# Kernel tuning notes

Hardware: AMD Instinct MI355X
Metric: run time of the kernel (lower is better)

Reference implementation:

```python
import jax, jax.numpy as jnp
import numpy as np

B, N, T, D, H = 8, 64, 256, 256, 8
HD = D // H


def _mlp(x, W1, b1, W2, b2):
    # torch nn.Sequential(Linear, GELU(exact), Linear); weights stored pre-transposed
    return jax.nn.gelu(x @ W1 + b1, approximate=False) @ W2 + b2


def setup_inputs() -> dict:
    key = jax.random.key(0)
    ks = jax.random.split(key, 14)
    s = 0.02
    f32 = jnp.float32
    return {
        "padded_batches": jax.random.normal(ks[0], (B, N, T, D), f32),
        "sum_token": jax.random.normal(ks[1], (B, N, 1, D), f32),
        "masks": jax.random.randint(ks[2], (B, N, T), 0, 2).astype(jnp.int32),
        "positions_3d": jax.random.normal(ks[3], (B, N, T, 3), f32),
        "Wq": jax.random.normal(ks[4], (D, D), f32) * s, "bq": jnp.zeros((D,), f32),
        "Wk": jax.random.normal(ks[5], (D, D), f32) * s, "bk": jnp.zeros((D,), f32),
        "Wv": jax.random.normal(ks[6], (D, D), f32) * s, "bv": jnp.zeros((D,), f32),
        "Bw1": jax.random.normal(ks[7], (5, 64), f32) * s, "Bb1": jnp.zeros((64,), f32),
        "Bw2": jax.random.normal(ks[8], (64, H), f32) * s, "Bb2": jnp.zeros((H,), f32),
        "Vw1": jax.random.normal(ks[9], (5, 128), f32) * s, "Vb1": jnp.zeros((128,), f32),
        "Vw2": jax.random.normal(ks[10], (128, D), f32) * s, "Vb2": jnp.zeros((D,), f32),
    }


def reference(padded_batches, sum_token, masks, positions_3d,
              Wq, bq, Wk, bk, Wv, bv,
              Bw1, Bb1, Bw2, Bb2, Vw1, Vb1, Vw2, Vb2):
    Bd, Nd, Td, Dd = padded_batches.shape
    BN = Bd * Nd
    # masked-average summary token (summary_mode='avg'): [B,N,1,D]
    w = masks[..., None].astype(padded_batches.dtype)            # [B,N,T,1]
    denom = jnp.clip(w.sum(-2, keepdims=True), 1e-6)
    summary = (padded_batches * w).sum(-2, keepdims=True) / denom
    # projections (torch Linear: x @ W.T + b; weights here pre-transposed)
    q = (padded_batches @ Wq + bq).reshape(BN, Td, H, HD).transpose(0, 2, 1, 3)  # [BN,H,T,Hd]
    k = (summary @ Wk + bk).reshape(BN, 1, H, HD).transpose(0, 2, 1, 3)          # [BN,H,1,Hd]
    v = (summary @ Wv + bv).reshape(BN, 1, H, HD).transpose(0, 2, 1, 3)
    scale = 1.0 / np.sqrt(HD).astype(np.float32)
    logits = jnp.einsum('bhtd,bhsd->bhts', q, k) * scale          # [BN,H,T,1]
    # relative positional features vs. position summary
    pos_summary = (positions_3d * w).sum(-2, keepdims=True) / denom  # [B,N,1,3]
    diff = positions_3d.reshape(BN, Td, 1, 3) - pos_summary.reshape(BN, 1, 1, 3)  # [BN,T,1,3]
    dist = jnp.linalg.norm(diff, axis=-1, keepdims=True)
    dist2 = (diff ** 2).sum(-1, keepdims=True)
    rel_feat = jnp.concatenate([diff, dist, dist2], axis=-1)      # [BN,T,1,5]
    rel_bias = _mlp(rel_feat, Bw1, Bb1, Bw2, Bb2).transpose(0, 3, 1, 2)  # [BN,H,T,1]
    logits = logits + rel_bias
    neg = jnp.finfo(jnp.float32).min
    attn_mask = jnp.where(masks.reshape(BN, 1, Td, 1) == 0, neg, 0.0)
    logits = logits + attn_mask
    attn_w = jax.nn.softmax(logits, axis=-1)                      # [BN,H,T,1]
    attn = jnp.einsum('bhts,bhsd->bhtd', attn_w, v)               # [BN,H,T,Hd]
    rel_val = _mlp(rel_feat, Vw1, Vb1, Vw2, Vb2)                  # [BN,T,1,D]
    rel_val = rel_val.reshape(BN, Td, 1, H, HD).transpose(0, 3, 1, 2, 4)  # [BN,H,T,1,Hd]
    attn = attn + (attn_w[..., None] * rel_val).sum(-2)
    out = attn.transpose(0, 2, 1, 3).reshape(Bd, Nd, Td, Dd) + padded_batches
    return out
```

## Files before the change

### kernel.cpp

```cpp
#include <hip/hip_runtime.h>
#include <hip/hip_bf16.h>
#include <math.h>


#define BN_TOT 512
#define T_DIM 256
#define D_DIM 256
#define HID 128

typedef __attribute__((ext_vector_type(8))) short short8v;
typedef __attribute__((ext_vector_type(4))) float f32x4;

static __device__ __forceinline__ ushort f2bf(float f) {
    __hip_bfloat16 h = __float2bfloat16(f);
    return *reinterpret_cast<ushort*>(&h);
}

__global__ __launch_bounds__(256) void k_prep(const float* __restrict__ Vw2,
                                              ushort* __restrict__ Vw2t) {
    const int idx = (blockIdx.x * 256 + threadIdx.x) * 4;
    const int d = idx >> 7, k = idx & 127;
    ushort4 r;
    r.x = f2bf(Vw2[(size_t)(k + 0) * D_DIM + d]);
    r.y = f2bf(Vw2[(size_t)(k + 1) * D_DIM + d]);
    r.z = f2bf(Vw2[(size_t)(k + 2) * D_DIM + d]);
    r.w = f2bf(Vw2[(size_t)(k + 3) * D_DIM + d]);
    *reinterpret_cast<ushort4*>(Vw2t + d * HID + k) = r;
}

__global__ __launch_bounds__(256, 8) void k_part(
    const float* __restrict__ x,
    const int* __restrict__ masks,
    const float* __restrict__ pos,
    float* __restrict__ part_x,
    float* __restrict__ part_cp)
{
    __shared__ float s_part[4 * 256];

    const int bid = blockIdx.x;
    const int tid = threadIdx.x;
    const int bn = bid >> 2, tg = bid & 3;
    const int t0 = tg * 64;

    const float* xb = x + ((size_t)bn * T_DIM + t0) * D_DIM;
    const int*   mb = masks + bn * T_DIM + t0;

    {
        const int dq = tid & 63, tq = tid >> 6;
        float4 a = make_float4(0.f, 0.f, 0.f, 0.f);
        #pragma unroll
        for (int i = 0; i < 16; ++i) {
            const int t = tq * 16 + i;
            float m = (float)mb[t];
            float4 xv = *reinterpret_cast<const float4*>(xb + (size_t)t * D_DIM + dq * 4);
            a.x += m * xv.x; a.y += m * xv.y; a.z += m * xv.z; a.w += m * xv.w;
        }
        *reinterpret_cast<float4*>(s_part + tq * 256 + dq * 4) = a;
    }

    if (tid < 64) {
        float m = (float)mb[tid];
        const float* pp = pos + ((size_t)bn * T_DIM + t0 + tid) * 3;
        float c = m, px = m * pp[0], py = m * pp[1], pz = m * pp[2];
        #pragma unroll
        for (int off = 32; off > 0; off >>= 1) {
            c  += __shfl_down(c,  off, 64);
            px += __shfl_down(px, off, 64);
            py += __shfl_down(py, off, 64);
            pz += __shfl_down(pz, off, 64);
        }
        if (tid == 0)
            *reinterpret_cast<float4*>(part_cp + (bn * 4 + tg) * 4) =
                make_float4(c, px, py, pz);
    }
    __syncthreads();

    float s = s_part[tid] + s_part[256 + tid] + s_part[512 + tid] + s_part[768 + tid];
    part_x[((size_t)bn * 4 + tg) * 256 + tid] = s;
}

__global__ __launch_bounds__(256, 8) void k_v(
    const float* __restrict__ part_x,
    const float* __restrict__ part_cp,
    const float* __restrict__ Wv,
    const float* __restrict__ bv,
    const float* __restrict__ Vb2,
    float* __restrict__ v_ws,
    float* __restrict__ ps_ws)
{
    __shared__ float s_sum[256];
    __shared__ float s_part[4 * 256];
    __shared__ float s_cp[16];

    const int bn = blockIdx.x, tid = threadIdx.x;

    if (tid < 16) s_cp[tid] = part_cp[bn * 16 + tid];
    const float* pb = part_x + (size_t)bn * 1024;
    float s = pb[tid] + pb[256 + tid] + pb[512 + tid] + pb[768 + tid];
    __syncthreads();

    const float cnt = s_cp[0] + s_cp[4] + s_cp[8] + s_cp[12];
    const float inv = 1.0f / fmaxf(cnt, 1e-6f);
    s_sum[tid] = s * inv;
    if (tid < 3) {
        float p = s_cp[tid + 1] + s_cp[tid + 5] + s_cp[tid + 9] + s_cp[tid + 13];
        ps_ws[bn * 4 + tid] = p * inv;
    }
    __syncthreads();

    {
        const int dq = tid & 63, kq = tid >> 6;
        float4 a = make_float4(0.f, 0.f, 0.f, 0.f);
        #pragma unroll 8
        for (int i = 0; i < 64; ++i) {
            const int k = kq * 64 + i;
            float sc = s_sum[k];
            float4 w = *reinterpret_cast<const float4*>(Wv + (size_t)k * D_DIM + dq * 4);
            a.x += sc * w.x; a.y += sc * w.y; a.z += sc * w.z; a.w += sc * w.w;
        }
        *reinterpret_cast<float4*>(s_part + kq * 256 + dq * 4) = a;
    }
    __syncthreads();
    v_ws[bn * D_DIM + tid] = s_part[tid] + s_part[256 + tid] + s_part[512 + tid] +
                             s_part[768 + tid] + bv[tid] + Vb2[tid];
}

__global__ __launch_bounds__(512, 8) void k_sum(
    const float* __restrict__ x, const int* __restrict__ masks,
    const float* __restrict__ pos, const float* __restrict__ Wv,
    const float* __restrict__ bv, const float* __restrict__ Vb2,
    float* __restrict__ v_ws, float* __restrict__ ps_ws)
{
    __shared__ float s_m[256];
    __shared__ float s_red[4 * 256];
    __shared__ float s_part[8 * 256];
    __shared__ float s_sum[256];

    const int bn = blockIdx.x, tid = threadIdx.x;
    const float* xb = x + (size_t)bn * T_DIM * D_DIM;

    if (tid < 256) {
        float m = (float)masks[bn * T_DIM + tid];
        s_m[tid] = m;
        const float* pp = pos + ((size_t)bn * T_DIM + tid) * 3;
        s_red[0 * 256 + tid] = m;
        s_red[1 * 256 + tid] = m * pp[0];
        s_red[2 * 256 + tid] = m * pp[1];
        s_red[3 * 256 + tid] = m * pp[2];
    }
    __syncthreads();
    {
        const int dq = tid & 63, tq = tid >> 6;
        float4 a = make_float4(0.f, 0.f, 0.f, 0.f);
        const float* px = xb + (size_t)tq * 32 * D_DIM + dq * 4;
        #pragma unroll 8
        for (int i = 0; i < 32; ++i) {
            float m = s_m[tq * 32 + i];
            float4 xv = *reinterpret_cast<const float4*>(px + i * D_DIM);
            a.x += m * xv.x; a.y += m * xv.y; a.z += m * xv.z; a.w += m * xv.w;
        }
        *reinterpret_cast<float4*>(s_part + tq * 256 + dq * 4) = a;
    }
    __syncthreads();
    for (int off = 128; off > 0; off >>= 1) {
        if (tid < off) {
            s_red[0 * 256 + tid] += s_red[0 * 256 + tid + off];
            s_red[1 * 256 + tid] += s_red[1 * 256 + tid + off];
            s_red[2 * 256 + tid] += s_red[2 * 256 + tid + off];
            s_red[3 * 256 + tid] += s_red[3 * 256 + tid + off];
        }
        __syncthreads();
    }
    const float inv = 1.0f / fmaxf(s_red[0], 1e-6f);
    if (tid < 3) ps_ws[bn * 4 + tid] = s_red[(tid + 1) * 256] * inv;
    if (tid < 256) {
        float s = 0.f;
        #pragma unroll
        for (int q = 0; q < 8; ++q) s += s_part[q * 256 + tid];
        s_sum[tid] = s * inv;
    }
    __syncthreads();
    {
        const int dq = tid & 63, kq = tid >> 6;
        float4 a = make_float4(0.f, 0.f, 0.f, 0.f);
        #pragma unroll 8
        for (int i = 0; i < 32; ++i) {
            const int k = kq * 32 + i;
            float sc = s_sum[k];
            float4 w = *reinterpret_cast<const float4*>(Wv + (size_t)k * D_DIM + dq * 4);
            a.x += sc * w.x; a.y += sc * w.y; a.z += sc * w.z; a.w += sc * w.w;
        }
        *reinterpret_cast<float4*>(s_part + kq * 256 + dq * 4) = a;
    }
    __syncthreads();
    if (tid < 256) {
        float r = bv[tid] + Vb2[tid];
        #pragma unroll
        for (int q = 0; q < 8; ++q) r += s_part[q * 256 + tid];
        v_ws[bn * D_DIM + tid] = r;
    }
}

__global__ __launch_bounds__(256, 4) void k_main(
    const float* __restrict__ x,
    const float* __restrict__ pos,
    const float* __restrict__ Vw1,
    const float* __restrict__ Vb1,
    const ushort* __restrict__ Vw2t,
    const float* __restrict__ v_ws,
    const float* __restrict__ ps_ws,
    float* __restrict__ out)
{
    __shared__ float s_rf[32 * 6];
    __shared__ __align__(16) float s_vb[256];
    __shared__ unsigned char s_hid[32 * HID * 2];

    const int tg  = blockIdx.x;
    const int bn  = blockIdx.y;
    const int tid = threadIdx.x;
    const int t0  = tg * 32;

    const int l  = tid & 63;
    const int wc = tid >> 6;

    const float* xb = x + ((size_t)bn * T_DIM + t0) * D_DIM;
    float4 xpre[2][4];
    #pragma unroll
    for (int m = 0; m < 2; ++m) {
        const int tok = m * 16 + (l & 15);
        #pragma unroll
        for (int n = 0; n < 4; ++n) {
            const int d0 = wc * 64 + n * 16 + ((l >> 4) << 2);
            xpre[m][n] = *reinterpret_cast<const float4*>(xb + (size_t)tok * D_DIM + d0);
        }
    }

    s_vb[tid] = v_ws[bn * D_DIM + tid];
    const float psx = ps_ws[bn * 4 + 0];
    const float psy = ps_ws[bn * 4 + 1];
    const float psz = ps_ws[bn * 4 + 2];
    if (tid < 32) {
        const float* pp = pos + ((size_t)bn * T_DIM + t0 + tid) * 3;
        float dx = pp[0] - psx, dy = pp[1] - psy, dz = pp[2] - psz;
        float d2 = dx * dx + dy * dy + dz * dz;
        s_rf[tid * 6 + 0] = dx; s_rf[tid * 6 + 1] = dy; s_rf[tid * 6 + 2] = dz;
        s_rf[tid * 6 + 3] = sqrtf(d2); s_rf[tid * 6 + 4] = d2;
    }
    __syncthreads();

    {
        const int cg = tid & 31;
        const int c0 = cg * 4;
        float wv0 = Vw1[0 * HID + c0], wv0b = Vw1[0 * HID + c0 + 1],
              wv0c = Vw1[0 * HID + c0 + 2], wv0d = Vw1[0 * HID + c0 + 3];
        float wv1 = Vw1[1 * HID + c0], wv1b = Vw1[1 * HID + c0 + 1],
              wv1c = Vw1[1 * HID + c0 + 2], wv1d = Vw1[1 * HID + c0 + 3];
        float wv2 = Vw1[2 * HID + c0], wv2b = Vw1[2 * HID + c0 + 1],
              wv2c = Vw1[2 * HID + c0 + 2], wv2d = Vw1[2 * HID + c0 + 3];
        float wv3 = Vw1[3 * HID + c0], wv3b = Vw1[3 * HID + c0 + 1],
              wv3c = Vw1[3 * HID + c0 + 2], wv3d = Vw1[3 * HID + c0 + 3];
        float wv4 = Vw1[4 * HID + c0], wv4b = Vw1[4 * HID + c0 + 1],
              wv4c = Vw1[4 * HID + c0 + 2], wv4d = Vw1[4 * HID + c0 + 3];
        float b0 = Vb1[c0], b1 = Vb1[c0 + 1], b2 = Vb1[c0 + 2], b3 = Vb1[c0 + 3];

        const int tok0 = (tid >> 5) * 4;
        #pragma unroll
        for (int s = 0; s < 4; ++s) {
            const int tok = tok0 + s;
            const float* rf = s_rf + tok * 6;
            const float dx = rf[0], dy = rf[1], dz = rf[2], dd = rf[3], d2 = rf[4];
            float z0 = b0 + dx * wv0 + dy * wv1 + dz * wv2 + dd * wv3 + d2 * wv4;
            float z1 = b1 + dx * wv0b + dy * wv1b + dz * wv2b + dd * wv3b + d2 * wv4b;
            float z2 = b2 + dx * wv0c + dy * wv1c + dz * wv2c + dd * wv3c + d2 * wv4c;
            float z3 = b3 + dx * wv0d + dy * wv1d + dz * wv2d + dd * wv3d + d2 * wv4d;
            float g0 = 0.5f * z0 * (1.0f + erff(z0 * 0.70710678118654752f));
            float g1 = 0.5f * z1 * (1.0f + erff(z1 * 0.70710678118654752f));
            float g2 = 0.5f * z2 * (1.0f + erff(z2 * 0.70710678118654752f));
            float g3 = 0.5f * z3 * (1.0f + erff(z3 * 0.70710678118654752f));
            uint p0 = (uint)f2bf(g0) | ((uint)f2bf(g1) << 16);
            uint p1 = (uint)f2bf(g2) | ((uint)f2bf(g3) << 16);
            int byte = tok * 256 + cg * 8;
            byte ^= (tok & 15) << 4;
            *reinterpret_cast<uint2*>(s_hid + byte) = make_uint2(p0, p1);
        }
    }
    __syncthreads();

    f32x4 acc[2][4];
    #pragma unroll
    for (int m = 0; m < 2; ++m)
        #pragma unroll
        for (int n = 0; n < 4; ++n) acc[m][n] = (f32x4){0.f, 0.f, 0.f, 0.f};

    const ushort* bbase = Vw2t + ((size_t)(wc * 64 + (l & 15))) * HID + ((l >> 4) * 8);
    const int koff16 = (l >> 4) * 16;

    #pragma unroll
    for (int ks = 0; ks < 4; ++ks) {
        short8v wfr[4];
        #pragma unroll
        for (int n = 0; n < 4; ++n)
            wfr[n] = *reinterpret_cast<const short8v*>(bbase + n * 16 * HID + ks * 32);
        short8v hfr[2];
        #pragma unroll
        for (int m = 0; m < 2; ++m) {
            const int tok = m * 16 + (l & 15);
            int byte = tok * 256 + ks * 64 + koff16;
            byte ^= (tok & 15) << 4;
            hfr[m] = *reinterpret_cast<const short8v*>(s_hid + byte);
        }
        #pragma unroll
        for (int m = 0; m < 2; ++m)
            #pragma unroll
            for (int n = 0; n < 4; ++n)
                acc[m][n] = __builtin_amdgcn_mfma_f32_16x16x32_bf16(
                    wfr[n], hfr[m], acc[m][n], 0, 0, 0);
    }

    #pragma unroll
    for (int m = 0; m < 2; ++m) {
        const int tok = m * 16 + (l & 15);
        float* orow = out + ((size_t)bn * T_DIM + t0 + tok) * D_DIM;
        #pragma unroll
        for (int n = 0; n < 4; ++n) {
            const int d0 = wc * 64 + n * 16 + ((l >> 4) << 2);
            float4 vb4 = *reinterpret_cast<const float4*>(s_vb + d0);
            float4 o;
            o.x = xpre[m][n].x + vb4.x + acc[m][n][0];
            o.y = xpre[m][n].y + vb4.y + acc[m][n][1];
            o.z = xpre[m][n].z + vb4.z + acc[m][n][2];
            o.w = xpre[m][n].w + vb4.w + acc[m][n][3];
            *reinterpret_cast<float4*>(orow + d0) = o;
        }
    }
}

extern "C" void kernel_launch(void* const* d_in, const int* in_sizes, int n_in,
                              void* d_out, int out_size, void* d_ws, size_t ws_size,
                              hipStream_t stream) {
    const float* x     = (const float*)d_in[0];
    const int*   masks = (const int*)d_in[2];
    const float* pos   = (const float*)d_in[3];
    const float* Wv    = (const float*)d_in[8];
    const float* bv    = (const float*)d_in[9];
    const float* Vw1   = (const float*)d_in[14];
    const float* Vb1   = (const float*)d_in[15];
    const float* Vw2   = (const float*)d_in[16];
    const float* Vb2   = (const float*)d_in[17];
    float* out = (float*)d_out;

    ushort* Vw2t  = (ushort*)d_ws;
    float*  v_ws  = (float*)(Vw2t + D_DIM * HID);
    float*  ps_ws = v_ws + BN_TOT * D_DIM;
    float*  part_x  = ps_ws + BN_TOT * 4;
    float*  part_cp = part_x + (size_t)BN_TOT * 4 * 256;
    const size_t need_main = (size_t)(part_cp + BN_TOT * 16 - (float*)d_ws) * 4;

    k_prep<<<32, 256, 0, stream>>>(Vw2, Vw2t);
    if (ws_size >= need_main) {
        k_part<<<BN_TOT * 4, 256, 0, stream>>>(x, masks, pos, part_x, part_cp);
        k_v<<<BN_TOT, 256, 0, stream>>>(part_x, part_cp, Wv, bv, Vb2, v_ws, ps_ws);
    } else {
        k_sum<<<BN_TOT, 512, 0, stream>>>(x, masks, pos, Wv, bv, Vb2, v_ws, ps_ws);
    }
    k_main<<<dim3(8, BN_TOT), 256, 0, stream>>>(x, pos, Vw1, Vb1, Vw2t,
                                                v_ws, ps_ws, out);
}
```

Measured before the change: 107.1 us.

## Loop k_main over four token tiles per block with tanh GELU and nontemporal IO

k_main now launches 1024 blocks, and each block processes four 32-token tiles of one bn in a loop. Per-block setup (v bias, position summary, Vw1 weights) is amortised across the tiles, and the next tile's x rows are prefetched after the current output is stored. Exact erf GELU is replaced by a tanh approximation built on __expf and a fast reciprocal, and x loads and out stores use nontemporal hints. The approximation changes numerics slightly, and the loop serialises work that previously ran across more blocks.

New measurement: 174.3 us. 62.8% more time.

```diff
diff --git a/kernel.cpp b/kernel.cpp
--- a/kernel.cpp
+++ b/kernel.cpp
@@ -14,6 +14,14 @@
 static __device__ __forceinline__ ushort f2bf(float f) {
     __hip_bfloat16 h = __float2bfloat16(f);
     return *reinterpret_cast<ushort*>(&h);
+}
+
+static __device__ __forceinline__ float gelu_fast(float z) {
+    float zc = fminf(z, 8.0f);
+    float u = 0.7978845608f * zc * (1.0f + 0.044715f * zc * zc);
+    float w = __expf(2.0f * u);
+    float t = (w - 1.0f) * __builtin_amdgcn_rcpf(w + 1.0f);
+    return 0.5f * z * (1.0f + t);
 }
 
 __global__ __launch_bounds__(256) void k_prep(const float* __restrict__ Vw2,
@@ -215,122 +223,130 @@
     __shared__ __align__(16) float s_vb[256];
     __shared__ unsigned char s_hid[32 * HID * 2];
 
-    const int tg  = blockIdx.x;
-    const int bn  = blockIdx.y;
+    const int b   = blockIdx.x;
+    const int bn  = b & (BN_TOT - 1);
+    const int tg0 = (b >> 9) * 4;
     const int tid = threadIdx.x;
-    const int t0  = tg * 32;
-
-    const int l  = tid & 63;
-    const int wc = tid >> 6;
-
-    const float* xb = x + ((size_t)bn * T_DIM + t0) * D_DIM;
-    float4 xpre[2][4];
-    #pragma unroll
-    for (int m = 0; m < 2; ++m) {
-        const int tok = m * 16 + (l & 15);
-        #pragma unroll
-        for (int n = 0; n < 4; ++n) {
-            const int d0 = wc * 64 + n * 16 + ((l >> 4) << 2);
-            xpre[m][n] = *reinterpret_cast<const float4*>(xb + (size_t)tok * D_DIM + d0);
-        }
-    }
+    const int l   = tid & 63;
+    const int wc  = tid >> 6;
 
     s_vb[tid] = v_ws[bn * D_DIM + tid];
     const float psx = ps_ws[bn * 4 + 0];
     const float psy = ps_ws[bn * 4 + 1];
     const float psz = ps_ws[bn * 4 + 2];
-    if (tid < 32) {
-        const float* pp = pos + ((size_t)bn * T_DIM + t0 + tid) * 3;
-        float dx = pp[0] - psx, dy = pp[1] - psy, dz = pp[2] - psz;
-        float d2 = dx * dx + dy * dy + dz * dz;
-        s_rf[tid * 6 + 0] = dx; s_rf[tid * 6 + 1] = dy; s_rf[tid * 6 + 2] = dz;
-        s_rf[tid * 6 + 3] = sqrtf(d2); s_rf[tid * 6 + 4] = d2;
-    }
-    __syncthreads();
-
-    {
-        const int cg = tid & 31;
-        const int c0 = cg * 4;
-        float wv0 = Vw1[0 * HID + c0], wv0b = Vw1[0 * HID + c0 + 1],
-              wv0c = Vw1[0 * HID + c0 + 2], wv0d = Vw1[0 * HID + c0 + 3];
-        float wv1 = Vw1[1 * HID + c0], wv1b = Vw1[1 * HID + c0 + 1],
-              wv1c = Vw1[1 * HID + c0 + 2], wv1d = Vw1[1 * HID + c0 + 3];
-        float wv2 = Vw1[2 * HID + c0], wv2b = Vw1[2 * HID + c0 + 1],
-              wv2c = Vw1[2 * HID + c0 + 2], wv2d = Vw1[2 * HID + c0 + 3];
-        float wv3 = Vw1[3 * HID + c0], wv3b = Vw1[3 * HID + c0 + 1],
-              wv3c = Vw1[3 * HID + c0 + 2], wv3d = Vw1[3 * HID + c0 + 3];
-        float wv4 = Vw1[4 * HID + c0], wv4b = Vw1[4 * HID + c0 + 1],
-              wv4c = Vw1[4 * HID + c0 + 2], wv4d = Vw1[4 * HID + c0 + 3];
-        float b0 = Vb1[c0], b1 = Vb1[c0 + 1], b2 = Vb1[c0 + 2], b3 = Vb1[c0 + 3];
-
-        const int tok0 = (tid >> 5) * 4;
-        #pragma unroll
-        for (int s = 0; s < 4; ++s) {
-            const int tok = tok0 + s;
-            const float* rf = s_rf + tok * 6;
-            const float dx = rf[0], dy = rf[1], dz = rf[2], dd = rf[3], d2 = rf[4];
-            float z0 = b0 + dx * wv0 + dy * wv1 + dz * wv2 + dd * wv3 + d2 * wv4;
-            float z1 = b1 + dx * wv0b + dy * wv1b + dz * wv2b + dd * wv3b + d2 * wv4b;
-            float z2 = b2 + dx * wv0c + dy * wv1c + dz * wv2c + dd * wv3c + d2 * wv4c;
-            float z3 = b3 + dx * wv0d + dy * wv1d + dz * wv2d + dd * wv3d + d2 * wv4d;
-            float g0 = 0.5f * z0 * (1.0f + erff(z0 * 0.70710678118654752f));
-            float g1 = 0.5f * z1 * (1.0f + erff(z1 * 0.70710678118654752f));
-            float g2 = 0.5f * z2 * (1.0f + erff(z2 * 0.70710678118654752f));
-            float g3 = 0.5f * z3 * (1.0f + erff(z3 * 0.70710678118654752f));
-            uint p0 = (uint)f2bf(g0) | ((uint)f2bf(g1) << 16);
-            uint p1 = (uint)f2bf(g2) | ((uint)f2bf(g3) << 16);
-            int byte = tok * 256 + cg * 8;
-            byte ^= (tok & 15) << 4;
-            *reinterpret_cast<uint2*>(s_hid + byte) = make_uint2(p0, p1);
-        }
-    }
-    __syncthreads();
-
-    f32x4 acc[2][4];
-    #pragma unroll
-    for (int m = 0; m < 2; ++m)
-        #pragma unroll
-        for (int n = 0; n < 4; ++n) acc[m][n] = (f32x4){0.f, 0.f, 0.f, 0.f};
-
+
+    const int cg = tid & 31, c0 = cg * 4;
+    const float4 w0 = *reinterpret_cast<const float4*>(Vw1 + 0 * HID + c0);
+    const float4 w1 = *reinterpret_cast<const float4*>(Vw1 + 1 * HID + c0);
+    const float4 w2 = *reinterpret_cast<const float4*>(Vw1 + 2 * HID + c0);
+    const float4 w3 = *reinterpret_cast<const float4*>(Vw1 + 3 * HID + c0);
+    const float4 w4 = *reinterpret_cast<const float4*>(Vw1 + 4 * HID + c0);
+    const float4 bb = *reinterpret_cast<const float4*>(Vb1 + c0);
+
+    const float* xbn = x + (size_t)bn * T_DIM * D_DIM;
     const ushort* bbase = Vw2t + ((size_t)(wc * 64 + (l & 15))) * HID + ((l >> 4) * 8);
     const int koff16 = (l >> 4) * 16;
 
+    f32x4 xpre[2][4];
     #pragma unroll
-    for (int ks = 0; ks < 4; ++ks) {
-        short8v wfr[4];
-        #pragma unroll
-        for (int n = 0; n < 4; ++n)
-            wfr[n] = *reinterpret_cast<const short8v*>(bbase + n * 16 * HID + ks * 32);
-        short8v hfr[2];
+    for (int m = 0; m < 2; ++m) {
+        const int tok = tg0 * 32 + m * 16 + (l & 15);
+        #pragma unroll
+        for (int n = 0; n < 4; ++n) {
+            const int d0 = wc * 64 + n * 16 + ((l >> 4) << 2);
+            xpre[m][n] = __builtin_nontemporal_load(
+                reinterpret_cast<const f32x4*>(xbn + (size_t)tok * D_DIM + d0));
+        }
+    }
+
+    #pragma unroll 1
+    for (int it = 0; it < 4; ++it) {
+        const int t0 = (tg0 + it) * 32;
+
+        if (tid < 32) {
+            const float* pp = pos + ((size_t)bn * T_DIM + t0 + tid) * 3;
+            float dx = pp[0] - psx, dy = pp[1] - psy, dz = pp[2] - psz;
+            float d2 = dx * dx + dy * dy + dz * dz;
+            s_rf[tid * 6 + 0] = dx; s_rf[tid * 6 + 1] = dy; s_rf[tid * 6 + 2] = dz;
+            s_rf[tid * 6 + 3] = sqrtf(d2); s_rf[tid * 6 + 4] = d2;
+        }
+        __syncthreads();
+
+        {
+            const int tok0 = (tid >> 5) * 4;
+            #pragma unroll
+            for (int s = 0; s < 4; ++s) {
+                const int tok = tok0 + s;
+                const float* rf = s_rf + tok * 6;
+                const float dx = rf[0], dy = rf[1], dz = rf[2], dd = rf[3], d2 = rf[4];
+                float z0 = bb.x + dx * w0.x + dy * w1.x + dz * w2.x + dd * w3.x + d2 * w4.x;
+                float z1 = bb.y + dx * w0.y + dy * w1.y + dz * w2.y + dd * w3.y + d2 * w4.y;
+                float z2 = bb.z + dx * w0.z + dy * w1.z + dz * w2.z + dd * w3.z + d2 * w4.z;
+                float z3 = bb.w + dx * w0.w + dy * w1.w + dz * w2.w + dd * w3.w + d2 * w4.w;
+                float g0 = gelu_fast(z0), g1 = gelu_fast(z1);
+                float g2 = gelu_fast(z2), g3 = gelu_fast(z3);
+                uint p0 = (uint)f2bf(g0) | ((uint)f2bf(g1) << 16);
+                uint p1 = (uint)f2bf(g2) | ((uint)f2bf(g3) << 16);
+                int byte = tok * 256 + cg * 8;
+                byte ^= (tok & 15) << 4;
+                *reinterpret_cast<uint2*>(s_hid + byte) = make_uint2(p0, p1);
+            }
+        }
+        __syncthreads();
+
+        f32x4 acc[2][4];
+        #pragma unroll
+        for (int m = 0; m < 2; ++m)
+            #pragma unroll
+            for (int n = 0; n < 4; ++n) acc[m][n] = (f32x4){0.f, 0.f, 0.f, 0.f};
+
+        #pragma unroll
+        for (int ks = 0; ks < 4; ++ks) {
+            short8v wfr[4];
+            #pragma unroll
+            for (int n = 0; n < 4; ++n)
+                wfr[n] = *reinterpret_cast<const short8v*>(bbase + n * 16 * HID + ks * 32);
+            short8v hfr[2];
+            #pragma unroll
+            for (int m = 0; m < 2; ++m) {
+                const int tok = m * 16 + (l & 15);
+                int byte = tok * 256 + ks * 64 + koff16;
+                byte ^= (tok & 15) << 4;
+                hfr[m] = *reinterpret_cast<const short8v*>(s_hid + byte);
+            }
+            #pragma unroll
+            for (int m = 0; m < 2; ++m)
+                #pragma unroll
+                for (int n = 0; n < 4; ++n)
+                    acc[m][n] = __builtin_amdgcn_mfma_f32_16x16x32_bf16(
+                        wfr[n], hfr[m], acc[m][n], 0, 0, 0);
+        }
+
         #pragma unroll
         for (int m = 0; m < 2; ++m) {
             const int tok = m * 16 + (l & 15);
-            int byte = tok * 256 + ks * 64 + koff16;
-            byte ^= (tok & 15) << 4;
-            hfr[m] = *reinterpret_cast<const short8v*>(s_hid + byte);
-        }
-        #pragma unroll
-        for (int m = 0; m < 2; ++m)
-            #pragma unroll
-            for (int n = 0; n < 4; ++n)
-                acc[m][n] = __builtin_amdgcn_mfma_f32_16x16x32_bf16(
-                    wfr[n], hfr[m], acc[m][n], 0, 0, 0);
-    }
-
-    #pragma unroll
-    for (int m = 0; m < 2; ++m) {
-        const int tok = m * 16 + (l & 15);
-        float* orow = out + ((size_t)bn * T_DIM + t0 + tok) * D_DIM;
-        #pragma unroll
-        for (int n = 0; n < 4; ++n) {
-            const int d0 = wc * 64 + n * 16 + ((l >> 4) << 2);
-            float4 vb4 = *reinterpret_cast<const float4*>(s_vb + d0);
-            float4 o;
-            o.x = xpre[m][n].x + vb4.x + acc[m][n][0];
-            o.y = xpre[m][n].y + vb4.y + acc[m][n][1];
-            o.z = xpre[m][n].z + vb4.z + acc[m][n][2];
-            o.w = xpre[m][n].w + vb4.w + acc[m][n][3];
-            *reinterpret_cast<float4*>(orow + d0) = o;
+            float* orow = out + ((size_t)bn * T_DIM + t0 + tok) * D_DIM;
+            #pragma unroll
+            for (int n = 0; n < 4; ++n) {
+                const int d0 = wc * 64 + n * 16 + ((l >> 4) << 2);
+                f32x4 vb4 = *reinterpret_cast<const f32x4*>(s_vb + d0);
+                f32x4 o = xpre[m][n] + vb4 + acc[m][n];
+                __builtin_nontemporal_store(o, reinterpret_cast<f32x4*>(orow + d0));
+            }
+        }
+
+        if (it < 3) {
+            const int t0n = (tg0 + it + 1) * 32;
+            #pragma unroll
+            for (int m = 0; m < 2; ++m) {
+                const int tok = t0n + m * 16 + (l & 15);
+                #pragma unroll
+                for (int n = 0; n < 4; ++n) {
+                    const int d0 = wc * 64 + n * 16 + ((l >> 4) << 2);
+                    xpre[m][n] = __builtin_nontemporal_load(
+                        reinterpret_cast<const f32x4*>(xbn + (size_t)tok * D_DIM + d0));
+                }
+            }
         }
     }
 }
@@ -363,6 +379,5 @@
     } else {
         k_sum<<<BN_TOT, 512, 0, stream>>>(x, masks, pos, Wv, bv, Vb2, v_ws, ps_ws);
     }
-    k_main<<<dim3(8, BN_TOT), 256, 0, stream>>>(x, pos, Vw1, Vb1, Vw2t,
-                                                v_ws, ps_ws, out);
-}
+    k_main<<<1024, 256, 0, stream>>>(x, pos, Vw1, Vb1, Vw2t, v_ws, ps_ws, out);
+}
```
